# Kernel optimization log

Hardware: AMD Instinct MI355X
Metric: run time of the kernel (lower is better)

## Reference

```python
import jax, jax.numpy as jnp
import numpy as np

D = 8      # data dim (output_size)
H = 512    # hidden size
B = 2048   # batch


def _masks(d, in_f, out_f):
    # block-diagonal mask (mask_d) and strictly-lower block mask (mask_o)
    md = np.zeros((out_f, in_f), np.float32)
    mo = np.zeros((out_f, in_f), np.float32)
    for i in range(d):
        md[i * out_f // d:(i + 1) * out_f // d, i * in_f // d:(i + 1) * in_f // d] = 1.0
        mo[i * out_f // d:(i + 1) * out_f // d, :(i + 1) * in_f // d] = 1.0
    return jnp.asarray(md), jnp.asarray(mo - md)


def _masked_linear(x, sld, W, logg, bias, d):
    out_f, in_f = W.shape
    md, mo = _masks(d, in_f, out_f)
    v = jnp.exp(W) * md + W * mo                       # weight-normalized masked weight
    v_norm = jnp.sqrt(jnp.sum(v * v, axis=1, keepdims=True))   # [out,1], L2 over in_features
    w = jnp.exp(logg) * v / v_norm
    out = x @ w.T + bias                               # [B,out]
    ld = logg + W - 0.5 * jnp.log(v_norm ** 2)         # [out,in]
    ob, ib = out_f // d, in_f // d
    # extract diagonal blocks (== tf.boolean_mask with mask_d, row-major)
    blocks = ld.reshape(d, ob, d, ib)[np.arange(d), :, np.arange(d), :]   # [d,ob,ib]
    ld_b = jnp.broadcast_to(blocks[None], (x.shape[0], d, ob, ib))        # tile to batch
    # sum_logdets: [.,d,prev_ob,1] -> transpose -> logsumexp accumulate
    sld = jax.nn.logsumexp(jnp.swapaxes(sld, -1, -2) + ld_b, axis=-1, keepdims=True)
    return out, sld


def _tanh(x, sld):
    ld = -2.0 * (x - jnp.log(2.0) + jax.nn.softplus(-2.0 * x))
    return jnp.tanh(x), sld + ld.reshape(sld.shape)


def _bnaf(x, params):
    d = x.shape[-1]
    sld = jnp.zeros((1, d, 1, 1), x.dtype)
    h = x
    for (W, g, b) in params:
        h, sld = _masked_linear(h, sld, W, g, b, d)
        h, sld = _tanh(h, sld)
    return h, jnp.squeeze(sld, (2, 3))


def setup_inputs() -> dict:
    key = jax.random.key(0)
    ks = jax.random.split(key, 13)
    inp = {"x": jax.random.normal(ks[0], (B, D), jnp.float32)}
    dims = [(D, H), (H, H), (H, H), (H, D)]  # (in_features, out_features)
    for j, (i_f, o_f) in enumerate(dims):
        inp[f"W{j+1}"] = jax.random.normal(ks[1 + 3 * j], (o_f, i_f), jnp.float32) * 0.1
        inp[f"logg{j+1}"] = jnp.log(jax.random.uniform(ks[2 + 3 * j], (o_f, 1), jnp.float32, 1e-3, 1.0))
        inp[f"bias{j+1}"] = jax.random.uniform(ks[3 + 3 * j], (o_f,), jnp.float32, -0.1, 0.1)
    return inp


def reference(x, W1, logg1, bias1, W2, logg2, bias2, W3, logg3, bias3, W4, logg4, bias4):
    params = [(W1, logg1, bias1), (W2, logg2, bias2), (W3, logg3, bias3), (W4, logg4, bias4)]
    return _bnaf(x, params)
```

## Files before the change

### kernel.cpp

```cpp
#include <hip/hip_runtime.h>
#include <hip/hip_bf16.h>
#include <math.h>

typedef unsigned short u16;
typedef short v8s __attribute__((ext_vector_type(8)));
typedef float v4f __attribute__((ext_vector_type(4)));

#define LN2F 0.69314718055994530942f

static constexpr size_t OFF_W1Q = 0;
static constexpr size_t OFF_W2Q = 32768;
static constexpr size_t OFF_W3Q = 557056;
static constexpr size_t OFF_W4Q = 1081344;
static constexpr size_t OFF_M1  = 1097728;
static constexpr size_t OFF_M2  = 1099776;
static constexpr size_t OFF_M3  = 1101824;
static constexpr size_t OFF_M4  = 1103872;
static constexpr size_t OFF_E2  = 1103936;
static constexpr size_t OFF_E3  = 1169472;
static constexpr size_t OFF_E4  = 1235008;

__device__ __forceinline__ u16 f2bf(float f) {
  __hip_bfloat16 h = __float2bfloat16(f);
  return *reinterpret_cast<u16*>(&h);
}
__device__ __forceinline__ float bf2f(u16 u) {
  union { unsigned int i; float f; } x; x.i = ((unsigned int)u) << 16; return x.f;
}

__global__ __launch_bounds__(256) void bnaf_prep(
    const float* __restrict__ W1, const float* __restrict__ lg1,
    const float* __restrict__ W2, const float* __restrict__ lg2,
    const float* __restrict__ W3, const float* __restrict__ lg3,
    const float* __restrict__ W4, const float* __restrict__ lg4,
    char* __restrict__ ws)
{
  const int row = blockIdx.x * 4 + (threadIdx.x >> 6);
  const int lane = threadIdx.x & 63;

  int layer, o, in_f, ibshift, RN;
  const float *W, *lg;
  u16* wq; float* marr; u16* E16 = nullptr; float* E32 = nullptr;
  if (row < 512)       { layer=1; o=row;      in_f=8;   ibshift=0; W=W1; lg=lg1; wq=(u16*)(ws+OFF_W1Q); marr=(float*)(ws+OFF_M1); RN=512; }
  else if (row < 1024) { layer=2; o=row-512;  in_f=512; ibshift=6; W=W2; lg=lg2; wq=(u16*)(ws+OFF_W2Q); marr=(float*)(ws+OFF_M2); E16=(u16*)(ws+OFF_E2); RN=512; }
  else if (row < 1536) { layer=3; o=row-1024; in_f=512; ibshift=6; W=W3; lg=lg3; wq=(u16*)(ws+OFF_W3Q); marr=(float*)(ws+OFF_M3); E16=(u16*)(ws+OFF_E3); RN=512; }
  else                 { layer=4; o=row-1536; in_f=512; ibshift=6; W=W4; lg=lg4; wq=(u16*)(ws+OFF_W4Q); marr=(float*)(ws+OFF_M4); E32=(float*)(ws+OFF_E4); RN=16; }
  const bool zero_row = (layer==4 && o >= 8);
  const int i = (layer==4) ? o : (o >> 6);

  float wr[8], vv[8];
  float acc = 0.f;
  #pragma unroll
  for (int k = 0; k < 8; ++k) {
    int c = lane + 64*k;
    float Wv = (!zero_row && c < in_f) ? W[o*in_f + c] : 0.f;
    wr[k] = Wv;
    int j = c >> ibshift;
    float v = (!zero_row && c < in_f) ? ((j==i) ? __expf(Wv) : (j < i ? Wv : 0.f)) : 0.f;
    vv[k] = v;
    acc += v*v;
  }
  #pragma unroll
  for (int d2 = 1; d2 < 64; d2 <<= 1) acc += __shfl_xor(acc, d2);
  const float vn  = sqrtf(acc);
  const float lvn = __logf(vn);
  const float lgo = zero_row ? 0.f : lg[o];
  const float scale = zero_row ? 0.f : (__expf(lgo) / vn);

  const int CH = (in_f < 32) ? 32 : in_f;
  #pragma unroll
  for (int k = 0; k < 8; ++k) {
    int c = lane + 64*k;
    if (c < CH)
      wq[((size_t)(c >> 5) * RN + o) * 32 + (c & 31)] = f2bf(vv[k] * scale);
  }
  float myldb = -INFINITY; int myjj = -1;
  #pragma unroll
  for (int k = 0; k < 8; ++k) {
    int c = lane + 64*k;
    if (!zero_row && c < in_f && (c >> ibshift) == i) {
      myldb = lgo + wr[k] - lvn;
      myjj  = c - (i << ibshift);
    }
  }
  float mm = myldb;
  #pragma unroll
  for (int d2 = 1; d2 < 64; d2 <<= 1) mm = fmaxf(mm, __shfl_xor(mm, d2));
  if (!zero_row) {
    if (lane == 0) marr[o] = mm;
    if (myjj >= 0) {
      float e = __expf(myldb - mm);
      if (E16) E16[o*64 + myjj] = f2bf(e);
      if (E32) E32[o*64 + myjj] = e;
    }
  }
}


template<int KT, int RN, int NT>
__device__ __forceinline__ void zphase(const u16* __restrict__ wq, const u16* hA,
                                       int ob0, int c16, int q, v4f* acc) {
  #pragma unroll
  for (int t = 0; t < NT; ++t) { v4f z = {0.f,0.f,0.f,0.f}; acc[t] = z; }
  #pragma unroll
  for (int kt = 0; kt < KT; ++kt) {
    v8s a = *(const v8s*)(hA + c16*520 + kt*32 + q*8);
    #pragma unroll
    for (int t = 0; t < NT; ++t) {
      v8s b = *(const v8s*)(wq + ((size_t)(kt*RN + ob0 + t*16 + c16)) * 32 + q*8);
      acc[t] = __builtin_amdgcn_mfma_f32_16x16x32_bf16(a, b, acc[t], 0, 0, 0);
    }
  }
}

__device__ __forceinline__ void zpost2(const v4f* acc, const float* __restrict__ bias,
                                       int ob0, int c16, int q,
                                       u16* hA, float tld[2][4]) {
  #pragma unroll
  for (int t = 0; t < 2; ++t) {
    int o = ob0 + t*16 + c16;
    float bi = bias[o];
    #pragma unroll
    for (int rg = 0; rg < 4; ++rg) {
      float z  = acc[t][rg] + bi;
      float t2 = 2.f*z;
      float e2 = __expf(-fabsf(t2));
      float th = copysignf(__fdividef(1.f - e2, 1.f + e2), z);
      float sp = fmaxf(-t2, 0.f) + __logf(1.f + e2);
      tld[t][rg] = -t2 + 2.f*LN2F - 2.f*sp;
      hA[(q*4 + rg)*520 + o] = f2bf(th);
    }
  }
}

__global__ __launch_bounds__(1024) void bnaf_main(
    const float* __restrict__ x,
    const float* __restrict__ b1, const float* __restrict__ b2,
    const float* __restrict__ b3, const float* __restrict__ b4,
    const char* __restrict__ ws, float* __restrict__ out)
{
  __shared__ u16 hA[16*520];
  __shared__ u16 sexp_s[8*16*72];
  __shared__ float pamax[16*16];
  __shared__ float amax_f[8*16];
  __shared__ float tld4_s[16*8];

  const u16* w1q = (const u16*)(ws + OFF_W1Q);
  const u16* w2q = (const u16*)(ws + OFF_W2Q);
  const u16* w3q = (const u16*)(ws + OFF_W3Q);
  const u16* w4q = (const u16*)(ws + OFF_W4Q);
  const float* m1 = (const float*)(ws + OFF_M1);
  const float* m2 = (const float*)(ws + OFF_M2);
  const float* m3 = (const float*)(ws + OFF_M3);
  const float* m4 = (const float*)(ws + OFF_M4);
  const u16* E2 = (const u16*)(ws + OFF_E2);
  const u16* E3 = (const u16*)(ws + OFF_E3);
  const float* E4 = (const float*)(ws + OFF_E4);

  const int tid = threadIdx.x;
  const int wv = tid >> 6, lane = tid & 63;
  const int c16 = lane & 15, q = lane >> 4;
  const int r0 = blockIdx.x * 16;
  const int pair = wv >> 1, half = wv & 1;
  const int ob0 = wv * 32;
  u16* sexp_p = sexp_s + pair * (16*72);

  if (tid < 512) {
    int r = tid >> 5, c = tid & 31;
    hA[r*520 + c] = f2bf((c < 8) ? x[(r0 + r)*8 + c] : 0.f);
  }
  __syncthreads();

  v4f acc[2];
  float tld[2][4], sld[2][4];

  zphase<1, 512, 2>(w1q, hA, ob0, c16, q, acc);
  __syncthreads();
  zpost2(acc, b1, ob0, c16, q, hA, tld);
  #pragma unroll
  for (int t = 0; t < 2; ++t) {
    float mv = m1[ob0 + t*16 + c16];
    #pragma unroll
    for (int rg = 0; rg < 4; ++rg) sld[t][rg] = mv + tld[t][rg];
  }
  __syncthreads();

  const u16* wqs[2] = {w2q, w3q};
  const float* bs[2] = {b2, b3};
  const float* ms[2] = {m2, m3};
  const u16* Es[2] = {E2, E3};
  #pragma unroll 1
  for (int L = 0; L < 2; ++L) {
    zphase<16, 512, 2>(wqs[L], hA, ob0, c16, q, acc);
    float pm[4];
    #pragma unroll
    for (int rg = 0; rg < 4; ++rg) {
      float v = fmaxf(sld[0][rg], sld[1][rg]);
      #pragma unroll
      for (int d2 = 1; d2 < 16; d2 <<= 1) v = fmaxf(v, __shfl_xor(v, d2));
      pm[rg] = v;
      pamax[wv*16 + q*4 + rg] = v;
    }
    __syncthreads();
    zpost2(acc, bs[L], ob0, c16, q, hA, tld);
    float am[4];
    #pragma unroll
    for (int rg = 0; rg < 4; ++rg)
      am[rg] = fmaxf(pm[rg], pamax[(wv^1)*16 + q*4 + rg]);
    #pragma unroll
    for (int t = 0; t < 2; ++t)
      #pragma unroll
      for (int rg = 0; rg < 4; ++rg)
        sexp_p[(q*4+rg)*72 + half*32 + t*16 + c16] = f2bf(__expf(sld[t][rg] - am[rg]));
    __syncthreads();
    v4f ea[2];
    #pragma unroll
    for (int t = 0; t < 2; ++t) { v4f z = {0.f,0.f,0.f,0.f}; ea[t] = z; }
    #pragma unroll
    for (int kt = 0; kt < 2; ++kt) {
      v8s a = *(const v8s*)(sexp_p + c16*72 + kt*32 + q*8);
      #pragma unroll
      for (int t = 0; t < 2; ++t) {
        v8s b = *(const v8s*)(Es[L] + (size_t)(ob0 + t*16 + c16) * 64 + kt*32 + q*8);
        ea[t] = __builtin_amdgcn_mfma_f32_16x16x32_bf16(a, b, ea[t], 0, 0, 0);
      }
    }
    #pragma unroll
    for (int t = 0; t < 2; ++t) {
      float mv = ms[L][ob0 + t*16 + c16];
      #pragma unroll
      for (int rg = 0; rg < 4; ++rg)
        sld[t][rg] = am[rg] + mv + __logf(ea[t][rg]) + tld[t][rg];
    }
  }

  zphase<16, 16, 1>(w4q, hA, 0, c16, q, acc);
  float pm4[4];
  #pragma unroll
  for (int rg = 0; rg < 4; ++rg) {
    float v = fmaxf(sld[0][rg], sld[1][rg]);
    #pragma unroll
    for (int d2 = 1; d2 < 16; d2 <<= 1) v = fmaxf(v, __shfl_xor(v, d2));
    pm4[rg] = v;
    pamax[wv*16 + q*4 + rg] = v;
  }
  if (wv == 0 && c16 < 8) {
    float bi = b4[c16];
    #pragma unroll
    for (int rg = 0; rg < 4; ++rg) {
      int r = q*4 + rg;
      float z  = acc[0][rg] + bi;
      float t2 = 2.f*z;
      float e2 = __expf(-fabsf(t2));
      float th = copysignf(__fdividef(1.f - e2, 1.f + e2), z);
      float sp = fmaxf(-t2, 0.f) + __logf(1.f + e2);
      tld4_s[r*8 + c16] = -t2 + 2.f*LN2F - 2.f*sp;
      out[(r0 + r)*8 + c16] = th;
    }
  }
  __syncthreads();
  {
    float am[4];
    #pragma unroll
    for (int rg = 0; rg < 4; ++rg) {
      am[rg] = fmaxf(pm4[rg], pamax[(wv^1)*16 + q*4 + rg]);
      amax_f[pair*16 + q*4 + rg] = am[rg];
    }
    #pragma unroll
    for (int t = 0; t < 2; ++t)
      #pragma unroll
      for (int rg = 0; rg < 4; ++rg)
        sexp_p[(q*4+rg)*72 + half*32 + t*16 + c16] = f2bf(__expf(sld[t][rg] - am[rg]));
  }
  __syncthreads();

  if (half == 0) {
    int r = c16, i = pair;
    float sum = 0.f;
    #pragma unroll
    for (int jj = 0; jj < 16; ++jj) {
      int j = q*16 + jj;
      sum += bf2f(sexp_p[r*72 + j]) * E4[i*64 + j];
    }
    sum += __shfl_xor(sum, 16);
    sum += __shfl_xor(sum, 32);
    float sldf = amax_f[i*16 + r] + m4[i] + __logf(sum) + tld4_s[r*8 + i];
    if (lane < 16) out[2048*8 + (r0 + r)*8 + i] = sldf;
  }
}

extern "C" void kernel_launch(void* const* d_in, const int* in_sizes, int n_in,
                              void* d_out, int out_size, void* d_ws, size_t ws_size,
                              hipStream_t stream) {
  const float* x   = (const float*)d_in[0];
  const float* W1  = (const float*)d_in[1];
  const float* lg1 = (const float*)d_in[2];
  const float* b1  = (const float*)d_in[3];
  const float* W2  = (const float*)d_in[4];
  const float* lg2 = (const float*)d_in[5];
  const float* b2  = (const float*)d_in[6];
  const float* W3  = (const float*)d_in[7];
  const float* lg3 = (const float*)d_in[8];
  const float* b3  = (const float*)d_in[9];
  const float* W4  = (const float*)d_in[10];
  const float* lg4 = (const float*)d_in[11];
  const float* b4  = (const float*)d_in[12];
  char* ws = (char*)d_ws;
  float* out = (float*)d_out;

  bnaf_prep<<<388, 256, 0, stream>>>(W1, lg1, W2, lg2, W3, lg3, W4, lg4, ws);
  bnaf_main<<<128, 1024, 0, stream>>>(x, b1, b2, b3, b4, ws, out);
}
```

Measured before the change: 116.0 us.

## Skip zero upper-triangular weight tiles and split last layer across waves

For the two hidden 512x512 layers, each wave now loops only over k-tiles up to its own diagonal block (ktmax = (pair+1)*2). The masked weights are zero above the block diagonal by construction, so those MFMAs and weight loads did no useful work. The final 512->8 layer was previously run with all 16 k-tiles by every wave. Now each wave computes one k-tile and writes its partial to a new shared buffer, and 256 threads sum the 16 partials before applying tanh and the log-det. This saves redundant MFMA and global-load work at the cost of load imbalance across waves, extra LDS space and one reduction step.

```diff
diff --git a/kernel.cpp b/kernel.cpp
--- a/kernel.cpp
+++ b/kernel.cpp
@@ -97,20 +97,33 @@
 }
 
 
-template<int KT, int RN, int NT>
-__device__ __forceinline__ void zphase(const u16* __restrict__ wq, const u16* hA,
-                                       int ob0, int c16, int q, v4f* acc) {
-  #pragma unroll
-  for (int t = 0; t < NT; ++t) { v4f z = {0.f,0.f,0.f,0.f}; acc[t] = z; }
-  #pragma unroll
-  for (int kt = 0; kt < KT; ++kt) {
-    v8s a = *(const v8s*)(hA + c16*520 + kt*32 + q*8);
-    #pragma unroll
-    for (int t = 0; t < NT; ++t) {
-      v8s b = *(const v8s*)(wq + ((size_t)(kt*RN + ob0 + t*16 + c16)) * 32 + q*8);
-      acc[t] = __builtin_amdgcn_mfma_f32_16x16x32_bf16(a, b, acc[t], 0, 0, 0);
-    }
-  }
+__device__ __forceinline__ void zphase_masked(const u16* __restrict__ wq, const u16* hA,
+                                              int ob0, int c16, int q, v4f acc[2], int ktmax) {
+  v4f z = {0.f,0.f,0.f,0.f}; acc[0] = z; acc[1] = z;
+  const u16* hrow  = hA + c16*520 + q*8;
+  const u16* wbase = wq + ((size_t)(ob0 + c16))*32 + q*8;
+  for (int kt = 0; kt < ktmax; kt += 2) {
+    v8s a0  = *(const v8s*)(hrow + kt*32);
+    v8s a1  = *(const v8s*)(hrow + kt*32 + 32);
+    v8s b00 = *(const v8s*)(wbase + (size_t)kt*512*32);
+    v8s b10 = *(const v8s*)(wbase + (size_t)kt*512*32 + 16*32);
+    v8s b01 = *(const v8s*)(wbase + (size_t)(kt+1)*512*32);
+    v8s b11 = *(const v8s*)(wbase + (size_t)(kt+1)*512*32 + 16*32);
+    acc[0] = __builtin_amdgcn_mfma_f32_16x16x32_bf16(a0, b00, acc[0], 0, 0, 0);
+    acc[1] = __builtin_amdgcn_mfma_f32_16x16x32_bf16(a0, b10, acc[1], 0, 0, 0);
+    acc[0] = __builtin_amdgcn_mfma_f32_16x16x32_bf16(a1, b01, acc[0], 0, 0, 0);
+    acc[1] = __builtin_amdgcn_mfma_f32_16x16x32_bf16(a1, b11, acc[1], 0, 0, 0);
+  }
+}
+
+__device__ __forceinline__ void zphase_l1(const u16* __restrict__ wq, const u16* hA,
+                                          int ob0, int c16, int q, v4f acc[2]) {
+  v4f z = {0.f,0.f,0.f,0.f}; acc[0] = z; acc[1] = z;
+  v8s a  = *(const v8s*)(hA + c16*520 + q*8);
+  v8s b0 = *(const v8s*)(wq + ((size_t)(ob0 + c16))*32 + q*8);
+  v8s b1 = *(const v8s*)(wq + ((size_t)(ob0 + 16 + c16))*32 + q*8);
+  acc[0] = __builtin_amdgcn_mfma_f32_16x16x32_bf16(a, b0, acc[0], 0, 0, 0);
+  acc[1] = __builtin_amdgcn_mfma_f32_16x16x32_bf16(a, b1, acc[1], 0, 0, 0);
 }
 
 __device__ __forceinline__ void zpost2(const v4f* acc, const float* __restrict__ bias,
@@ -141,6 +154,7 @@
 {
   __shared__ u16 hA[16*520];
   __shared__ u16 sexp_s[8*16*72];
+  __shared__ float pacc_s[16*260];
   __shared__ float pamax[16*16];
   __shared__ float amax_f[8*16];
   __shared__ float tld4_s[16*8];
@@ -163,6 +177,7 @@
   const int r0 = blockIdx.x * 16;
   const int pair = wv >> 1, half = wv & 1;
   const int ob0 = wv * 32;
+  const int ktmax = (pair + 1) * 2;
   u16* sexp_p = sexp_s + pair * (16*72);
 
   if (tid < 512) {
@@ -174,7 +189,7 @@
   v4f acc[2];
   float tld[2][4], sld[2][4];
 
-  zphase<1, 512, 2>(w1q, hA, ob0, c16, q, acc);
+  zphase_l1(w1q, hA, ob0, c16, q, acc);
   __syncthreads();
   zpost2(acc, b1, ob0, c16, q, hA, tld);
   #pragma unroll
@@ -191,7 +206,7 @@
   const u16* Es[2] = {E2, E3};
   #pragma unroll 1
   for (int L = 0; L < 2; ++L) {
-    zphase<16, 512, 2>(wqs[L], hA, ob0, c16, q, acc);
+    zphase_masked(wqs[L], hA, ob0, c16, q, acc, ktmax);
     float pm[4];
     #pragma unroll
     for (int rg = 0; rg < 4; ++rg) {
@@ -234,7 +249,13 @@
     }
   }
 
-  zphase<16, 16, 1>(w4q, hA, 0, c16, q, acc);
+  {
+    v8s a = *(const v8s*)(hA + c16*520 + wv*32 + q*8);
+    v8s b = *(const v8s*)(w4q + ((size_t)(wv*16 + c16))*32 + q*8);
+    v4f z4 = {0.f,0.f,0.f,0.f};
+    z4 = __builtin_amdgcn_mfma_f32_16x16x32_bf16(a, b, z4, 0, 0, 0);
+    *(v4f*)(pacc_s + wv*260 + lane*4) = z4;
+  }
   float pm4[4];
   #pragma unroll
   for (int rg = 0; rg < 4; ++rg) {
@@ -244,21 +265,24 @@
     pm4[rg] = v;
     pamax[wv*16 + q*4 + rg] = v;
   }
-  if (wv == 0 && c16 < 8) {
-    float bi = b4[c16];
-    #pragma unroll
-    for (int rg = 0; rg < 4; ++rg) {
-      int r = q*4 + rg;
-      float z  = acc[0][rg] + bi;
+  __syncthreads();
+
+  if (tid < 256) {
+    int s = tid, rg = s & 3, l = s >> 2;
+    int c = l & 15, qq = l >> 4, r = qq*4 + rg;
+    float z = 0.f;
+    #pragma unroll
+    for (int w = 0; w < 16; ++w) z += pacc_s[w*260 + s];
+    if (c < 8) {
+      z += b4[c];
       float t2 = 2.f*z;
       float e2 = __expf(-fabsf(t2));
       float th = copysignf(__fdividef(1.f - e2, 1.f + e2), z);
       float sp = fmaxf(-t2, 0.f) + __logf(1.f + e2);
-      tld4_s[r*8 + c16] = -t2 + 2.f*LN2F - 2.f*sp;
-      out[(r0 + r)*8 + c16] = th;
-    }
-  }
-  __syncthreads();
+      tld4_s[r*8 + c] = -t2 + 2.f*LN2F - 2.f*sp;
+      out[(r0 + r)*8 + c] = th;
+    }
+  }
   {
     float am[4];
     #pragma unroll
```

Result: faster. 108.4 us (-6.6%).

## Skip zero blocks in masked GEMMs and balance triangular work across waves

Applied to the files above, without the earlier changes.

Each wave now owns output tiles t and 31-t and iterates only over the nonzero lower-triangular K blocks of the masked weight, so the per-wave K loops are complementary lengths and the total work stays even across waves. hA is double-buffered, which removes one barrier per layer, and weight and E tiles are prefetched ahead of use. The max-subtraction in the logsumexp is dropped, so exp(sld) is taken directly, which risks overflow or underflow for large log-dets. The final layer splits K across waves with a shared-memory reduction.

```diff
diff --git a/kernel.cpp b/kernel.cpp
--- a/kernel.cpp
+++ b/kernel.cpp
@@ -97,38 +97,48 @@
 }
 
 
-template<int KT, int RN, int NT>
-__device__ __forceinline__ void zphase(const u16* __restrict__ wq, const u16* hA,
-                                       int ob0, int c16, int q, v4f* acc) {
-  #pragma unroll
-  for (int t = 0; t < NT; ++t) { v4f z = {0.f,0.f,0.f,0.f}; acc[t] = z; }
-  #pragma unroll
-  for (int kt = 0; kt < KT; ++kt) {
-    v8s a = *(const v8s*)(hA + c16*520 + kt*32 + q*8);
-    #pragma unroll
-    for (int t = 0; t < NT; ++t) {
-      v8s b = *(const v8s*)(wq + ((size_t)(kt*RN + ob0 + t*16 + c16)) * 32 + q*8);
-      acc[t] = __builtin_amdgcn_mfma_f32_16x16x32_bf16(a, b, acc[t], 0, 0, 0);
-    }
-  }
-}
-
-__device__ __forceinline__ void zpost2(const v4f* acc, const float* __restrict__ bias,
-                                       int ob0, int c16, int q,
-                                       u16* hA, float tld[2][4]) {
-  #pragma unroll
-  for (int t = 0; t < 2; ++t) {
-    int o = ob0 + t*16 + c16;
-    float bi = bias[o];
-    #pragma unroll
-    for (int rg = 0; rg < 4; ++rg) {
-      float z  = acc[t][rg] + bi;
+__device__ __forceinline__ void zphase2(const u16* __restrict__ wq, const u16* hA,
+                                        int t0, int t1, int K0, int K1,
+                                        int c16, int q, v4f acc[2], v8s bp0, v8s bp1) {
+  const u16* hrow = hA + c16*520 + q*8;
+  const u16* wb0  = wq + ((size_t)(t0*16 + c16))*32 + q*8;
+  const u16* wb1  = wq + ((size_t)(t1*16 + c16))*32 + q*8;
+  v4f z = {0.f,0.f,0.f,0.f};
+  v8s a0 = *(const v8s*)(hrow);
+  acc[0] = __builtin_amdgcn_mfma_f32_16x16x32_bf16(a0, bp0, z, 0, 0, 0);
+  acc[1] = __builtin_amdgcn_mfma_f32_16x16x32_bf16(a0, bp1, z, 0, 0, 0);
+  int kt = 1;
+  for (; kt < K0; ++kt) {
+    v8s a  = *(const v8s*)(hrow + kt*32);
+    v8s b0 = *(const v8s*)(wb0 + (size_t)kt*512*32);
+    v8s b1 = *(const v8s*)(wb1 + (size_t)kt*512*32);
+    acc[0] = __builtin_amdgcn_mfma_f32_16x16x32_bf16(a, b0, acc[0], 0, 0, 0);
+    acc[1] = __builtin_amdgcn_mfma_f32_16x16x32_bf16(a, b1, acc[1], 0, 0, 0);
+  }
+  for (; kt < K1; ++kt) {
+    v8s a  = *(const v8s*)(hrow + kt*32);
+    v8s b1 = *(const v8s*)(wb1 + (size_t)kt*512*32);
+    acc[1] = __builtin_amdgcn_mfma_f32_16x16x32_bf16(a, b1, acc[1], 0, 0, 0);
+  }
+}
+
+__device__ __forceinline__ void zpost2(const v4f* acc, float bi0, float bi1,
+                                       int t0, int t1, int c16, int q,
+                                       u16* hout, float tld[2][4]) {
+  const float bi[2] = {bi0, bi1};
+  const int   tt[2] = {t0, t1};
+  #pragma unroll
+  for (int s = 0; s < 2; ++s) {
+    int o = tt[s]*16 + c16;
+    #pragma unroll
+    for (int rg = 0; rg < 4; ++rg) {
+      float z  = acc[s][rg] + bi[s];
       float t2 = 2.f*z;
       float e2 = __expf(-fabsf(t2));
       float th = copysignf(__fdividef(1.f - e2, 1.f + e2), z);
       float sp = fmaxf(-t2, 0.f) + __logf(1.f + e2);
-      tld[t][rg] = -t2 + 2.f*LN2F - 2.f*sp;
-      hA[(q*4 + rg)*520 + o] = f2bf(th);
+      tld[s][rg] = -t2 + 2.f*LN2F - 2.f*sp;
+      hout[(q*4 + rg)*520 + o] = f2bf(th);
     }
   }
 }
@@ -139,11 +149,12 @@
     const float* __restrict__ b3, const float* __restrict__ b4,
     const char* __restrict__ ws, float* __restrict__ out)
 {
-  __shared__ u16 hA[16*520];
-  __shared__ u16 sexp_s[8*16*72];
-  __shared__ float pamax[16*16];
-  __shared__ float amax_f[8*16];
-  __shared__ float tld4_s[16*8];
+  __shared__ u16 hA0[16*520];
+  __shared__ u16 hA1[16*520];
+  __shared__ u16 sexp_s[8*16*64];
+
+  float* pacc = (float*)hA0;
+  float* tld4 = (float*)hA1;
 
   const u16* w1q = (const u16*)(ws + OFF_W1Q);
   const u16* w2q = (const u16*)(ws + OFF_W2Q);
@@ -161,130 +172,145 @@
   const int wv = tid >> 6, lane = tid & 63;
   const int c16 = lane & 15, q = lane >> 4;
   const int r0 = blockIdx.x * 16;
-  const int pair = wv >> 1, half = wv & 1;
-  const int ob0 = wv * 32;
-  u16* sexp_p = sexp_s + pair * (16*72);
+  const int t0 = wv, t1 = 31 - wv;
+  const int blk0 = wv >> 2, blk1 = 7 - blk0;
+  const int K0 = 2*(blk0 + 1), K1 = 2*(blk1 + 1);
+
+  v8s b1p0 = *(const v8s*)(w1q + ((size_t)(t0*16 + c16))*32 + q*8);
+  v8s b1p1 = *(const v8s*)(w1q + ((size_t)(t1*16 + c16))*32 + q*8);
+  float m1v0 = m1[t0*16 + c16], m1v1 = m1[t1*16 + c16];
+  float b1v0 = b1[t0*16 + c16], b1v1 = b1[t1*16 + c16];
 
   if (tid < 512) {
     int r = tid >> 5, c = tid & 31;
-    hA[r*520 + c] = f2bf((c < 8) ? x[(r0 + r)*8 + c] : 0.f);
+    hA0[r*520 + c] = f2bf((c < 8) ? x[(r0 + r)*8 + c] : 0.f);
   }
   __syncthreads();
 
   v4f acc[2];
   float tld[2][4], sld[2][4];
 
-  zphase<1, 512, 2>(w1q, hA, ob0, c16, q, acc);
+  { v8s a = *(const v8s*)(hA0 + c16*520 + q*8);
+    v4f z = {0.f,0.f,0.f,0.f};
+    acc[0] = __builtin_amdgcn_mfma_f32_16x16x32_bf16(a, b1p0, z, 0, 0, 0);
+    acc[1] = __builtin_amdgcn_mfma_f32_16x16x32_bf16(a, b1p1, z, 0, 0, 0); }
+  v8s bp0 = *(const v8s*)(w2q + ((size_t)(t0*16 + c16))*32 + q*8);
+  v8s bp1 = *(const v8s*)(w2q + ((size_t)(t1*16 + c16))*32 + q*8);
+  zpost2(acc, b1v0, b1v1, t0, t1, c16, q, hA1, tld);
+  #pragma unroll
+  for (int rg = 0; rg < 4; ++rg) {
+    sld[0][rg] = m1v0 + tld[0][rg];
+    sld[1][rg] = m1v1 + tld[1][rg];
+  }
   __syncthreads();
-  zpost2(acc, b1, ob0, c16, q, hA, tld);
-  #pragma unroll
-  for (int t = 0; t < 2; ++t) {
-    float mv = m1[ob0 + t*16 + c16];
-    #pragma unroll
-    for (int rg = 0; rg < 4; ++rg) sld[t][rg] = mv + tld[t][rg];
-  }
+
+  {
+    v8s e00 = *(const v8s*)(E2 + (size_t)(t0*16+c16)*64 + q*8);
+    v8s e01 = *(const v8s*)(E2 + (size_t)(t0*16+c16)*64 + 32 + q*8);
+    v8s e10 = *(const v8s*)(E2 + (size_t)(t1*16+c16)*64 + q*8);
+    v8s e11 = *(const v8s*)(E2 + (size_t)(t1*16+c16)*64 + 32 + q*8);
+    float mv0 = m2[t0*16+c16], mv1 = m2[t1*16+c16];
+    float bv0 = b2[t0*16+c16], bv1 = b2[t1*16+c16];
+    zphase2(w2q, hA1, t0, t1, K0, K1, c16, q, acc, bp0, bp1);
+    bp0 = *(const v8s*)(w3q + ((size_t)(t0*16 + c16))*32 + q*8);
+    bp1 = *(const v8s*)(w3q + ((size_t)(t1*16 + c16))*32 + q*8);
+    zpost2(acc, bv0, bv1, t0, t1, c16, q, hA0, tld);
+    #pragma unroll
+    for (int rg = 0; rg < 4; ++rg) {
+      sexp_s[blk0*1024 + (q*4+rg)*64 + (t0&3)*16 + c16] = f2bf(__expf(sld[0][rg]));
+      sexp_s[blk1*1024 + (q*4+rg)*64 + (t1&3)*16 + c16] = f2bf(__expf(sld[1][rg]));
+    }
+    __syncthreads();
+    v4f ea0 = {0.f,0.f,0.f,0.f}, ea1 = {0.f,0.f,0.f,0.f};
+    { v8s a0 = *(const v8s*)(sexp_s + blk0*1024 + c16*64 + q*8);
+      v8s a1 = *(const v8s*)(sexp_s + blk1*1024 + c16*64 + q*8);
+      ea0 = __builtin_amdgcn_mfma_f32_16x16x32_bf16(a0, e00, ea0, 0, 0, 0);
+      ea1 = __builtin_amdgcn_mfma_f32_16x16x32_bf16(a1, e10, ea1, 0, 0, 0);
+      a0 = *(const v8s*)(sexp_s + blk0*1024 + c16*64 + 32 + q*8);
+      a1 = *(const v8s*)(sexp_s + blk1*1024 + c16*64 + 32 + q*8);
+      ea0 = __builtin_amdgcn_mfma_f32_16x16x32_bf16(a0, e01, ea0, 0, 0, 0);
+      ea1 = __builtin_amdgcn_mfma_f32_16x16x32_bf16(a1, e11, ea1, 0, 0, 0); }
+    #pragma unroll
+    for (int rg = 0; rg < 4; ++rg) {
+      sld[0][rg] = mv0 + __logf(ea0[rg]) + tld[0][rg];
+      sld[1][rg] = mv1 + __logf(ea1[rg]) + tld[1][rg];
+    }
+  }
+
+  v8s bw4;
+  {
+    v8s e00 = *(const v8s*)(E3 + (size_t)(t0*16+c16)*64 + q*8);
+    v8s e01 = *(const v8s*)(E3 + (size_t)(t0*16+c16)*64 + 32 + q*8);
+    v8s e10 = *(const v8s*)(E3 + (size_t)(t1*16+c16)*64 + q*8);
+    v8s e11 = *(const v8s*)(E3 + (size_t)(t1*16+c16)*64 + 32 + q*8);
+    float mv0 = m3[t0*16+c16], mv1 = m3[t1*16+c16];
+    float bv0 = b3[t0*16+c16], bv1 = b3[t1*16+c16];
+    zphase2(w3q, hA0, t0, t1, K0, K1, c16, q, acc, bp0, bp1);
+    bw4 = *(const v8s*)(w4q + ((size_t)(wv*16 + c16))*32 + q*8);
+    zpost2(acc, bv0, bv1, t0, t1, c16, q, hA1, tld);
+    __syncthreads();
+    #pragma unroll
+    for (int rg = 0; rg < 4; ++rg) {
+      sexp_s[blk0*1024 + (q*4+rg)*64 + (t0&3)*16 + c16] = f2bf(__expf(sld[0][rg]));
+      sexp_s[blk1*1024 + (q*4+rg)*64 + (t1&3)*16 + c16] = f2bf(__expf(sld[1][rg]));
+    }
+    __syncthreads();
+    v4f ea0 = {0.f,0.f,0.f,0.f}, ea1 = {0.f,0.f,0.f,0.f};
+    { v8s a0 = *(const v8s*)(sexp_s + blk0*1024 + c16*64 + q*8);
+      v8s a1 = *(const v8s*)(sexp_s + blk1*1024 + c16*64 + q*8);
+      ea0 = __builtin_amdgcn_mfma_f32_16x16x32_bf16(a0, e00, ea0, 0, 0, 0);
+      ea1 = __builtin_amdgcn_mfma_f32_16x16x32_bf16(a1, e10, ea1, 0, 0, 0);
+      a0 = *(const v8s*)(sexp_s + blk0*1024 + c16*64 + 32 + q*8);
+      a1 = *(const v8s*)(sexp_s + blk1*1024 + c16*64 + 32 + q*8);
+      ea0 = __builtin_amdgcn_mfma_f32_16x16x32_bf16(a0, e01, ea0, 0, 0, 0);
+      ea1 = __builtin_amdgcn_mfma_f32_16x16x32_bf16(a1, e11, ea1, 0, 0, 0); }
+    #pragma unroll
+    for (int rg = 0; rg < 4; ++rg) {
+      sld[0][rg] = mv0 + __logf(ea0[rg]) + tld[0][rg];
+      sld[1][rg] = mv1 + __logf(ea1[rg]) + tld[1][rg];
+    }
+  }
+
+  { v8s a = *(const v8s*)(hA1 + c16*520 + wv*32 + q*8);
+    v4f z = {0.f,0.f,0.f,0.f};
+    v4f z4 = __builtin_amdgcn_mfma_f32_16x16x32_bf16(a, bw4, z, 0, 0, 0);
+    *(v4f*)(pacc + wv*256 + lane*4) = z4; }
   __syncthreads();
 
-  const u16* wqs[2] = {w2q, w3q};
-  const float* bs[2] = {b2, b3};
-  const float* ms[2] = {m2, m3};
-  const u16* Es[2] = {E2, E3};
-  #pragma unroll 1
-  for (int L = 0; L < 2; ++L) {
-    zphase<16, 512, 2>(wqs[L], hA, ob0, c16, q, acc);
-    float pm[4];
-    #pragma unroll
-    for (int rg = 0; rg < 4; ++rg) {
-      float v = fmaxf(sld[0][rg], sld[1][rg]);
-      #pragma unroll
-      for (int d2 = 1; d2 < 16; d2 <<= 1) v = fmaxf(v, __shfl_xor(v, d2));
-      pm[rg] = v;
-      pamax[wv*16 + q*4 + rg] = v;
-    }
-    __syncthreads();
-    zpost2(acc, bs[L], ob0, c16, q, hA, tld);
-    float am[4];
-    #pragma unroll
-    for (int rg = 0; rg < 4; ++rg)
-      am[rg] = fmaxf(pm[rg], pamax[(wv^1)*16 + q*4 + rg]);
-    #pragma unroll
-    for (int t = 0; t < 2; ++t)
-      #pragma unroll
-      for (int rg = 0; rg < 4; ++rg)
-        sexp_p[(q*4+rg)*72 + half*32 + t*16 + c16] = f2bf(__expf(sld[t][rg] - am[rg]));
-    __syncthreads();
-    v4f ea[2];
-    #pragma unroll
-    for (int t = 0; t < 2; ++t) { v4f z = {0.f,0.f,0.f,0.f}; ea[t] = z; }
-    #pragma unroll
-    for (int kt = 0; kt < 2; ++kt) {
-      v8s a = *(const v8s*)(sexp_p + c16*72 + kt*32 + q*8);
-      #pragma unroll
-      for (int t = 0; t < 2; ++t) {
-        v8s b = *(const v8s*)(Es[L] + (size_t)(ob0 + t*16 + c16) * 64 + kt*32 + q*8);
-        ea[t] = __builtin_amdgcn_mfma_f32_16x16x32_bf16(a, b, ea[t], 0, 0, 0);
-      }
-    }
-    #pragma unroll
-    for (int t = 0; t < 2; ++t) {
-      float mv = ms[L][ob0 + t*16 + c16];
-      #pragma unroll
-      for (int rg = 0; rg < 4; ++rg)
-        sld[t][rg] = am[rg] + mv + __logf(ea[t][rg]) + tld[t][rg];
-    }
-  }
-
-  zphase<16, 16, 1>(w4q, hA, 0, c16, q, acc);
-  float pm4[4];
   #pragma unroll
   for (int rg = 0; rg < 4; ++rg) {
-    float v = fmaxf(sld[0][rg], sld[1][rg]);
-    #pragma unroll
-    for (int d2 = 1; d2 < 16; d2 <<= 1) v = fmaxf(v, __shfl_xor(v, d2));
-    pm4[rg] = v;
-    pamax[wv*16 + q*4 + rg] = v;
-  }
-  if (wv == 0 && c16 < 8) {
-    float bi = b4[c16];
-    #pragma unroll
-    for (int rg = 0; rg < 4; ++rg) {
-      int r = q*4 + rg;
-      float z  = acc[0][rg] + bi;
+    sexp_s[blk0*1024 + (q*4+rg)*64 + (t0&3)*16 + c16] = f2bf(__expf(sld[0][rg]));
+    sexp_s[blk1*1024 + (q*4+rg)*64 + (t1&3)*16 + c16] = f2bf(__expf(sld[1][rg]));
+  }
+  if (tid < 256) {
+    int s = tid, rg = s & 3, l = s >> 2;
+    int c = l & 15, qq = l >> 4, r = qq*4 + rg;
+    float z = 0.f;
+    #pragma unroll
+    for (int w = 0; w < 16; ++w) z += pacc[w*256 + s];
+    if (c < 8) {
+      z += b4[c];
       float t2 = 2.f*z;
       float e2 = __expf(-fabsf(t2));
       float th = copysignf(__fdividef(1.f - e2, 1.f + e2), z);
       float sp = fmaxf(-t2, 0.f) + __logf(1.f + e2);
-      tld4_s[r*8 + c16] = -t2 + 2.f*LN2F - 2.f*sp;
-      out[(r0 + r)*8 + c16] = th;
+      tld4[r*8 + c] = -t2 + 2.f*LN2F - 2.f*sp;
+      out[(r0 + r)*8 + c] = th;
     }
   }
   __syncthreads();
-  {
-    float am[4];
-    #pragma unroll
-    for (int rg = 0; rg < 4; ++rg) {
-      am[rg] = fmaxf(pm4[rg], pamax[(wv^1)*16 + q*4 + rg]);
-      amax_f[pair*16 + q*4 + rg] = am[rg];
-    }
-    #pragma unroll
-    for (int t = 0; t < 2; ++t)
-      #pragma unroll
-      for (int rg = 0; rg < 4; ++rg)
-        sexp_p[(q*4+rg)*72 + half*32 + t*16 + c16] = f2bf(__expf(sld[t][rg] - am[rg]));
-  }
-  __syncthreads();
-
-  if (half == 0) {
-    int r = c16, i = pair;
+
+  if (wv < 8) {
+    int r = c16, i = wv;
     float sum = 0.f;
     #pragma unroll
     for (int jj = 0; jj < 16; ++jj) {
       int j = q*16 + jj;
-      sum += bf2f(sexp_p[r*72 + j]) * E4[i*64 + j];
+      sum += bf2f(sexp_s[i*1024 + r*64 + j]) * E4[i*64 + j];
     }
     sum += __shfl_xor(sum, 16);
     sum += __shfl_xor(sum, 32);
-    float sldf = amax_f[i*16 + r] + m4[i] + __logf(sum) + tld4_s[r*8 + i];
+    float sldf = m4[i] + __logf(sum) + tld4[r*8 + i];
     if (lane < 16) out[2048*8 + (r0 + r)*8 + i] = sldf;
   }
 }
```

After: 103.1 us. 1.13x faster.
